# Kernel tuning notes

Hardware: AMD Instinct MI355X
Metric: run time of the kernel (lower is better)

Reference implementation:

```python
import jax, jax.numpy as jnp
import numpy as np

EPS = 1e-7
B, F, C, H, W, D = 2, 2, 64, 32, 104, 96


def _pix_homog(h, w):
    ys, xs = jnp.meshgrid(jnp.arange(h, dtype=jnp.float32),
                          jnp.arange(w, dtype=jnp.float32), indexing='ij')
    return jnp.stack([xs.ravel(), ys.ravel(), jnp.ones(h * w, jnp.float32)], 0)  # [3, H*W]


def setup_inputs() -> dict:
    key = jax.random.key(0)
    k1, k2 = jax.random.split(key)
    current_feats = jax.random.normal(k1, (B, C, H, W), jnp.float32)
    lookup_feats = jax.random.normal(k2, (B, F, C, H, W), jnp.float32)

    rng = np.random.RandomState(0)
    # intrinsics at matching (feature) resolution, monodepth2-style
    Km = np.eye(4, dtype=np.float32)
    Km[0, 0] = 0.58 * W
    Km[1, 1] = 1.92 * H
    Km[0, 2] = 0.5 * W
    Km[1, 2] = 0.5 * H
    K = np.tile(Km[None], (B, 1, 1))
    invK = np.linalg.inv(K).astype(np.float32)

    # near-identity relative poses (small rotation perturbation + small translation)
    poses = np.tile(np.eye(4, dtype=np.float32)[None, None], (B, F, 1, 1))
    poses[:, :, :3, :3] += 0.02 * rng.randn(B, F, 3, 3).astype(np.float32)
    poses[:, :, :3, 3] = 0.1 * rng.randn(B, F, 3).astype(np.float32)

    depth_bins = jnp.linspace(0.1, 20.0, D, dtype=jnp.float32)
    return {
        'current_feats': current_feats,
        'lookup_feats': lookup_feats,
        'poses': jnp.asarray(poses),
        'K': jnp.asarray(K),
        'invK': jnp.asarray(invK),
        'depth_bins': depth_bins,
    }


def _grid_sample_zeros(lfT, gx, gy, h, w):
    """Bilinear grid_sample, align_corners=True, padding_mode='zeros'.
    lfT: [B,F,H,W,C]; gx,gy: [B,F,D,H,W] in pixel coords. -> [B,F,D,H,W,C]"""
    x0 = jnp.floor(gx)
    y0 = jnp.floor(gy)
    x0i = x0.astype(jnp.int32)
    y0i = y0.astype(jnp.int32)
    wx1 = gx - x0
    wy1 = gy - y0
    wx0 = 1.0 - wx1
    wy0 = 1.0 - wy1
    bb = jnp.arange(lfT.shape[0])[:, None, None, None, None]
    ff = jnp.arange(lfT.shape[1])[None, :, None, None, None]

    def corner(yi, xi, wgt):
        m = ((xi >= 0) & (xi < w) & (yi >= 0) & (yi < h)).astype(lfT.dtype)
        xc = jnp.clip(xi, 0, w - 1)
        yc = jnp.clip(yi, 0, h - 1)
        v = lfT[bb, ff, yc, xc]                      # [B,F,D,H,W,C]
        return v * (m * wgt)[..., None]

    return (corner(y0i, x0i, wy0 * wx0) + corner(y0i, x0i + 1, wy0 * wx1)
            + corner(y0i + 1, x0i, wy1 * wx0) + corner(y0i + 1, x0i + 1, wy1 * wx1))


def reference(current_feats, lookup_feats, poses, K, invK, depth_bins):
    b, c, h, w = current_feats.shape
    f = lookup_feats.shape[1]
    d = depth_bins.shape[0]

    # Backproject: world points for each hypothesised depth plane
    pix = _pix_homog(h, w)                                   # [3, HW]
    cam = jnp.einsum('bij,jn->bin', invK[:, :3, :3], pix)    # [B,3,HW]
    pts = depth_bins[None, :, None, None] * cam[:, None]     # [B,D,3,HW]
    world = jnp.concatenate([pts, jnp.ones((b, d, 1, h * w), pts.dtype)], 2)  # [B,D,4,HW]

    # Project into each lookup frame
    P = jnp.einsum('bij,bfjk->bfik', K, poses)[:, :, :3, :]  # [B,F,3,4]
    cpts = jnp.einsum('bfij,bdjn->bfdin', P, world)          # [B,F,D,3,HW]
    xy = cpts[:, :, :, :2] / (cpts[:, :, :, 2:3] + EPS)      # pixel coords [B,F,D,2,HW]
    xy = xy.reshape(b, f, d, 2, h, w)
    gx, gy = xy[:, :, :, 0], xy[:, :, :, 1]                  # [B,F,D,H,W]

    # edge mask (detach in original -> stop_gradient)
    sx, sy = jax.lax.stop_gradient(gx), jax.lax.stop_gradient(gy)
    edge = ((sx >= 2.0) & (sx <= w - 2) & (sy >= 2.0) & (sy <= h - 2)).astype(jnp.float32)
    interior = jnp.zeros((h, w), jnp.float32).at[2:-2, 2:-2].set(1.0)
    edge_mask = edge * interior                               # [B,F,D,H,W]

    # warp lookup features and L1-diff against current features
    lfT = lookup_feats.transpose(0, 1, 3, 4, 2)               # [B,F,H,W,C]
    warped = _grid_sample_zeros(lfT, gx, gy, h, w)            # [B,F,D,H,W,C]
    cur = current_feats.transpose(0, 2, 3, 1)                 # [B,H,W,C]
    diffs = jnp.abs(warped - cur[:, None, None]).mean(-1) * edge_mask  # [B,F,D,H,W]

    # skip lookup frames whose pose is all-zero
    valid = (poses.sum((-2, -1)) != 0).astype(jnp.float32)    # [B,F]
    diffs = diffs * valid[:, :, None, None, None]

    cost = diffs.sum(1)                                        # [B,D,H,W]
    counts = (diffs > 0).astype(jnp.float32).sum(1)
    cost = cost / (counts + EPS)

    # set missing values to per-pixel max over depth bins
    missing = (cost == 0.0)
    cmax = cost.max(1, keepdims=True)
    cost = jnp.where(missing, cmax, cost)
    return cost
```

## Files before the change

### kernel.cpp

```cpp
#include <hip/hip_runtime.h>
#include <math.h>

constexpr int B_ = 2, F_ = 2, C_ = 64, H_ = 32, W_ = 104, D_ = 96;
constexpr int HW_ = H_ * W_;
#define EPSF 1e-7f

constexpr size_t LFT_OFF  = 0;
constexpr size_t CURT_OFF = LFT_OFF + (size_t)B_ * F_ * HW_ * C_;

constexpr int NT_BLKS = (HW_ / 32) * (C_ / 32) * (B_ * F_ + B_);
constexpr int DCH = 8;

__global__ __launch_bounds__(256) void prep_kernel(
        const float* __restrict__ cur, const float* __restrict__ lf,
        float* __restrict__ ws) {
    __shared__ float tile[32][33];
    int bid = blockIdx.x;
    int slice = bid / 208;
    int rem   = bid % 208;
    int nb = rem % 104, cb = rem / 104;
    const float* inS;
    float* outS;
    if (slice < B_ * F_) {
        inS  = lf + (size_t)slice * C_ * HW_;
        outS = ws + LFT_OFF + (size_t)slice * HW_ * C_;
    } else {
        int s2 = slice - B_ * F_;
        inS  = cur + (size_t)s2 * C_ * HW_;
        outS = ws + CURT_OFF + (size_t)s2 * HW_ * C_;
    }
    int t = threadIdx.x;
    int tx = t & 31, ty = t >> 5;
    int n0 = nb * 32, c0 = cb * 32;
    #pragma unroll
    for (int k = 0; k < 32; k += 8)
        tile[ty + k][tx] = inS[(size_t)(c0 + ty + k) * HW_ + n0 + tx];
    __syncthreads();
    #pragma unroll
    for (int k = 0; k < 32; k += 8)
        outS[(size_t)(n0 + ty + k) * C_ + c0 + tx] = tile[tx][ty + k];
}

__global__ __launch_bounds__(128) void sample_kernel(
        const float* __restrict__ poses, const float* __restrict__ K,
        const float* __restrict__ invK, const float* __restrict__ depth_bins,
        const float* __restrict__ ws, float* __restrict__ out) {
    int t   = threadIdx.x;
    int bid = blockIdx.x;
    int xt  = bid % 13;  int r = bid / 13;
    int d0c = r % (D_ / DCH);  r /= (D_ / DCH);
    int y   = r % H_;
    int b   = r / H_;
    int d0  = d0c * DCH;

    if (y < 2 || y >= H_ - 2) {
        if (t < 8 * DCH) {
            int dd = t >> 3, p2 = t & 7;
            out[((size_t)(b * D_ + d0 + dd) * H_ + y) * W_ + xt * 8 + p2] = 0.0f;
        }
        return;
    }

    __shared__ float2 gls[F_][DCH][8];

    {
        int px = t & 7, dc = (t >> 3) & 7, f = t >> 6;
        int x = xt * 8 + px, d = d0 + dc;
        const float* Kb   = K + (size_t)b * 16;
        const float* pose = poses + (size_t)(b * F_ + f) * 16;
        float P[12];
        #pragma unroll
        for (int i = 0; i < 3; ++i) {
            #pragma unroll
            for (int k = 0; k < 4; ++k) {
                float acc = __fmul_rn(Kb[i*4+0], pose[0*4+k]);
                acc = __fmaf_rn(Kb[i*4+1], pose[1*4+k], acc);
                acc = __fmaf_rn(Kb[i*4+2], pose[2*4+k], acc);
                acc = __fmaf_rn(Kb[i*4+3], pose[3*4+k], acc);
                P[i*4+k] = acc;
            }
        }
        float vs = 0.f;
        #pragma unroll
        for (int j = 0; j < 16; ++j) vs += pose[j];
        bool valid = (vs != 0.f);

        const float* iK = invK + (size_t)b * 16;
        float xf = (float)x, yf = (float)y;
        float cam0 = __fmul_rn(iK[0], xf); cam0 = __fmaf_rn(iK[1], yf, cam0); cam0 = __fmaf_rn(iK[2],  1.0f, cam0);
        float cam1 = __fmul_rn(iK[4], xf); cam1 = __fmaf_rn(iK[5], yf, cam1); cam1 = __fmaf_rn(iK[6],  1.0f, cam1);
        float cam2 = __fmul_rn(iK[8], xf); cam2 = __fmaf_rn(iK[9], yf, cam2); cam2 = __fmaf_rn(iK[10], 1.0f, cam2);
        float depth = depth_bins[d];
        float p0 = __fmul_rn(depth, cam0);
        float p1 = __fmul_rn(depth, cam1);
        float p2 = __fmul_rn(depth, cam2);

        float c0 = __fmul_rn(P[0], p0); c0 = __fmaf_rn(P[1], p1, c0); c0 = __fmaf_rn(P[2],  p2, c0); c0 = __fmaf_rn(P[3],  1.0f, c0);
        float c1 = __fmul_rn(P[4], p0); c1 = __fmaf_rn(P[5], p1, c1); c1 = __fmaf_rn(P[6],  p2, c1); c1 = __fmaf_rn(P[7],  1.0f, c1);
        float c2 = __fmul_rn(P[8], p0); c2 = __fmaf_rn(P[9], p1, c2); c2 = __fmaf_rn(P[10], p2, c2); c2 = __fmaf_rn(P[11], 1.0f, c2);
        float denom = __fadd_rn(c2, EPSF);
        float gx = c0 / denom;
        float gy = c1 / denom;

        bool interior = (x >= 2) && (x <= W_ - 3);
        bool m = valid && interior && (gx >= 2.0f) && (gx <= (float)(W_ - 2))
                                   && (gy >= 2.0f) && (gy <= (float)(H_ - 2));
        gls[f][dc][px] = m ? make_float2(gx, gy) : make_float2(2.0f, -1.0f);
    }
    __syncthreads();

    int lane = t & 15, px = t >> 4;
    int x = xt * 8 + px;
    const float4 cv = *(const float4*)(ws + CURT_OFF
                        + ((size_t)((b * H_ + y) * W_ + x)) * C_ + lane * 4);
    const float* lf0 = ws + LFT_OFF + (size_t)(b * F_ + 0) * HW_ * C_ + lane * 4;
    const float* lf1 = ws + LFT_OFF + (size_t)(b * F_ + 1) * HW_ * C_ + lane * 4;

    #pragma unroll 4
    for (int dc = 0; dc < DCH; ++dc) {
        float costsum = 0.f, counts = 0.f;
        #pragma unroll
        for (int f = 0; f < F_; ++f) {
            float2 g = gls[f][dc][px];
            bool  m  = (g.y >= 0.f);
            float gyv = m ? g.y : 2.0f;
            float gxv = g.x;
            float x0f = floorf(gxv), y0f = floorf(gyv);
            int   x0  = (int)x0f,    y0  = (int)y0f;
            float wx1 = gxv - x0f, wy1 = gyv - y0f;
            float wx0 = 1.f - wx1, wy0 = 1.f - wy1;
            float w00 = wy0 * wx0, w01 = wy0 * wx1, w10 = wy1 * wx0, w11 = wy1 * wx1;
            const float* bp = (f == 0 ? lf0 : lf1) + (size_t)(y0 * W_ + x0) * C_;
            float4 v00 = *(const float4*)(bp);
            float4 v01 = *(const float4*)(bp + C_);
            float4 v10 = *(const float4*)(bp + W_ * C_);
            float4 v11 = *(const float4*)(bp + W_ * C_ + C_);
            float s;
            s  = fabsf(v00.x*w00 + v01.x*w01 + v10.x*w10 + v11.x*w11 - cv.x);
            s += fabsf(v00.y*w00 + v01.y*w01 + v10.y*w10 + v11.y*w11 - cv.y);
            s += fabsf(v00.z*w00 + v01.z*w01 + v10.z*w10 + v11.z*w11 - cv.z);
            s += fabsf(v00.w*w00 + v01.w*w01 + v10.w*w10 + v11.w*w11 - cv.w);
            s += __shfl_xor(s, 1);
            s += __shfl_xor(s, 2);
            s += __shfl_xor(s, 4);
            s += __shfl_xor(s, 8);
            float diff = __fmul_rn(s, 1.0f / 64.0f) * (m ? 1.0f : 0.0f);
            costsum += diff;
            counts  += (diff > 0.f) ? 1.0f : 0.0f;
        }
        float cost = costsum / __fadd_rn(counts, EPSF);
        if (lane == 0)
            out[((size_t)(b * D_ + d0 + dc) * H_ + y) * W_ + x] = cost;
    }
}

__global__ __launch_bounds__(128) void fix_kernel(float* __restrict__ out) {
    int t  = threadIdx.x;
    int px = t & 7, j = t >> 3;
    int colg = blockIdx.x * 8 + px;
    int b  = colg / HW_;
    int yx = colg % HW_;
    float* base = out + (size_t)b * D_ * HW_ + yx;
    float v[6];
    float pm = 0.f;
    #pragma unroll
    for (int k = 0; k < 6; ++k) {
        v[k] = base[(size_t)(j + 16 * k) * HW_];
        pm = fmaxf(pm, v[k]);
    }
    __shared__ float pmbuf[128];
    __shared__ float cmaxbuf[8];
    pmbuf[t] = pm;
    __syncthreads();
    if (t < 8) {
        float cm = 0.f;
        #pragma unroll
        for (int jj = 0; jj < 16; ++jj) cm = fmaxf(cm, pmbuf[jj * 8 + t]);
        cmaxbuf[t] = cm;
    }
    __syncthreads();
    float cm = cmaxbuf[px];
    #pragma unroll
    for (int k = 0; k < 6; ++k)
        base[(size_t)(j + 16 * k) * HW_] = (v[k] == 0.0f) ? cm : v[k];
}

extern "C" void kernel_launch(void* const* d_in, const int* in_sizes, int n_in,
                              void* d_out, int out_size, void* d_ws, size_t ws_size,
                              hipStream_t stream) {
    const float* cur        = (const float*)d_in[0];
    const float* lf         = (const float*)d_in[1];
    const float* poses      = (const float*)d_in[2];
    const float* K          = (const float*)d_in[3];
    const float* invK       = (const float*)d_in[4];
    const float* depth_bins = (const float*)d_in[5];
    float* out = (float*)d_out;
    float* ws  = (float*)d_ws;

    prep_kernel<<<NT_BLKS, 256, 0, stream>>>(cur, lf, ws);

    int sample_blocks = B_ * H_ * 13 * (D_ / DCH);
    sample_kernel<<<sample_blocks, 128, 0, stream>>>(poses, K, invK, depth_bins, ws, out);

    fix_kernel<<<(B_ * HW_) / 8, 128, 0, stream>>>(out);
}
```

Baseline: 113.4 us.

## Fuse sampling and max-fill into one kernel covering all depth bins per block

Merges the sampling and fix kernels so each block handles all 96 depth bins for 8 pixels in a row. Sample offsets and bilinear weights are computed once into shared memory, the per-pixel max over depth is taken from a shared cost buffer, and the output is written once, so the separate read-modify-write pass over the output goes away. Corner loads are skipped when the integer sample offset repeats across consecutive depths. In exchange there are far fewer blocks (832 instead of 9984), which lowers parallelism and latency hiding, and each thread walks a serial 48-step depth loop.

```diff
diff --git a/kernel.cpp b/kernel.cpp
--- a/kernel.cpp
+++ b/kernel.cpp
@@ -9,7 +9,6 @@
 constexpr size_t CURT_OFF = LFT_OFF + (size_t)B_ * F_ * HW_ * C_;
 
 constexpr int NT_BLKS = (HW_ / 32) * (C_ / 32) * (B_ * F_ + B_);
-constexpr int DCH = 8;
 
 __global__ __launch_bounds__(256) void prep_kernel(
         const float* __restrict__ cur, const float* __restrict__ lf,
@@ -41,31 +40,32 @@
         outS[(size_t)(n0 + ty + k) * C_ + c0 + tx] = tile[tx][ty + k];
 }
 
-__global__ __launch_bounds__(128) void sample_kernel(
+__global__ __launch_bounds__(256) void mega_kernel(
         const float* __restrict__ poses, const float* __restrict__ K,
         const float* __restrict__ invK, const float* __restrict__ depth_bins,
         const float* __restrict__ ws, float* __restrict__ out) {
     int t   = threadIdx.x;
     int bid = blockIdx.x;
     int xt  = bid % 13;  int r = bid / 13;
-    int d0c = r % (D_ / DCH);  r /= (D_ / DCH);
     int y   = r % H_;
     int b   = r / H_;
-    int d0  = d0c * DCH;
 
     if (y < 2 || y >= H_ - 2) {
-        if (t < 8 * DCH) {
-            int dd = t >> 3, p2 = t & 7;
-            out[((size_t)(b * D_ + d0 + dd) * H_ + y) * W_ + xt * 8 + p2] = 0.0f;
+        for (int k = t; k < 8 * D_; k += 256) {
+            int d = k >> 3, px = k & 7;
+            out[((size_t)(b * D_ + d) * H_ + y) * W_ + xt * 8 + px] = 0.0f;
         }
         return;
     }
 
-    __shared__ float2 gls[F_][DCH][8];
-
-    {
-        int px = t & 7, dc = (t >> 3) & 7, f = t >> 6;
-        int x = xt * 8 + px, d = d0 + dc;
+    __shared__ int   offs[F_][D_][8];
+    __shared__ float wts [F_][D_][8][4];
+    __shared__ float costb[8][D_];
+    __shared__ float pmax[32][8];
+    __shared__ float cmaxb[8];
+
+    #pragma unroll
+    for (int f = 0; f < F_; ++f) {
         const float* Kb   = K + (size_t)b * 16;
         const float* pose = poses + (size_t)(b * F_ + f) * 16;
         float P[12];
@@ -84,105 +84,130 @@
         #pragma unroll
         for (int j = 0; j < 16; ++j) vs += pose[j];
         bool valid = (vs != 0.f);
-
         const float* iK = invK + (size_t)b * 16;
-        float xf = (float)x, yf = (float)y;
-        float cam0 = __fmul_rn(iK[0], xf); cam0 = __fmaf_rn(iK[1], yf, cam0); cam0 = __fmaf_rn(iK[2],  1.0f, cam0);
-        float cam1 = __fmul_rn(iK[4], xf); cam1 = __fmaf_rn(iK[5], yf, cam1); cam1 = __fmaf_rn(iK[6],  1.0f, cam1);
-        float cam2 = __fmul_rn(iK[8], xf); cam2 = __fmaf_rn(iK[9], yf, cam2); cam2 = __fmaf_rn(iK[10], 1.0f, cam2);
-        float depth = depth_bins[d];
-        float p0 = __fmul_rn(depth, cam0);
-        float p1 = __fmul_rn(depth, cam1);
-        float p2 = __fmul_rn(depth, cam2);
-
-        float c0 = __fmul_rn(P[0], p0); c0 = __fmaf_rn(P[1], p1, c0); c0 = __fmaf_rn(P[2],  p2, c0); c0 = __fmaf_rn(P[3],  1.0f, c0);
-        float c1 = __fmul_rn(P[4], p0); c1 = __fmaf_rn(P[5], p1, c1); c1 = __fmaf_rn(P[6],  p2, c1); c1 = __fmaf_rn(P[7],  1.0f, c1);
-        float c2 = __fmul_rn(P[8], p0); c2 = __fmaf_rn(P[9], p1, c2); c2 = __fmaf_rn(P[10], p2, c2); c2 = __fmaf_rn(P[11], 1.0f, c2);
-        float denom = __fadd_rn(c2, EPSF);
-        float gx = c0 / denom;
-        float gy = c1 / denom;
-
-        bool interior = (x >= 2) && (x <= W_ - 3);
-        bool m = valid && interior && (gx >= 2.0f) && (gx <= (float)(W_ - 2))
-                                   && (gy >= 2.0f) && (gy <= (float)(H_ - 2));
-        gls[f][dc][px] = m ? make_float2(gx, gy) : make_float2(2.0f, -1.0f);
+
+        #pragma unroll
+        for (int k = 0; k < 3; ++k) {
+            int idx = t + 256 * k;
+            int dd = idx >> 3, px = idx & 7;
+            int x = xt * 8 + px;
+            float xf = (float)x, yf = (float)y;
+            float cam0 = __fmul_rn(iK[0], xf); cam0 = __fmaf_rn(iK[1], yf, cam0); cam0 = __fmaf_rn(iK[2],  1.0f, cam0);
+            float cam1 = __fmul_rn(iK[4], xf); cam1 = __fmaf_rn(iK[5], yf, cam1); cam1 = __fmaf_rn(iK[6],  1.0f, cam1);
+            float cam2 = __fmul_rn(iK[8], xf); cam2 = __fmaf_rn(iK[9], yf, cam2); cam2 = __fmaf_rn(iK[10], 1.0f, cam2);
+            float depth = depth_bins[dd];
+            float p0 = __fmul_rn(depth, cam0);
+            float p1 = __fmul_rn(depth, cam1);
+            float p2 = __fmul_rn(depth, cam2);
+            float c0 = __fmul_rn(P[0], p0); c0 = __fmaf_rn(P[1], p1, c0); c0 = __fmaf_rn(P[2],  p2, c0); c0 = __fmaf_rn(P[3],  1.0f, c0);
+            float c1 = __fmul_rn(P[4], p0); c1 = __fmaf_rn(P[5], p1, c1); c1 = __fmaf_rn(P[6],  p2, c1); c1 = __fmaf_rn(P[7],  1.0f, c1);
+            float c2 = __fmul_rn(P[8], p0); c2 = __fmaf_rn(P[9], p1, c2); c2 = __fmaf_rn(P[10], p2, c2); c2 = __fmaf_rn(P[11], 1.0f, c2);
+            float denom = __fadd_rn(c2, EPSF);
+            float gx = c0 / denom;
+            float gy = c1 / denom;
+            bool interior = (x >= 2) && (x <= W_ - 3);
+            bool m = valid && interior && (gx >= 2.0f) && (gx <= (float)(W_ - 2))
+                                       && (gy >= 2.0f) && (gy <= (float)(H_ - 2));
+            if (m) {
+                float x0f = floorf(gx), y0f = floorf(gy);
+                int   x0  = (int)x0f,   y0  = (int)y0f;
+                float wx1 = gx - x0f, wy1 = gy - y0f;
+                float wx0 = 1.f - wx1, wy0 = 1.f - wy1;
+                wts[f][dd][px][0] = wy0 * wx0;
+                wts[f][dd][px][1] = wy0 * wx1;
+                wts[f][dd][px][2] = wy1 * wx0;
+                wts[f][dd][px][3] = wy1 * wx1;
+                offs[f][dd][px] = (y0 * W_ + x0) * C_;
+            } else {
+                offs[f][dd][px] = -1;
+                wts[f][dd][px][0] = 0.f;
+                wts[f][dd][px][1] = 0.f;
+                wts[f][dd][px][2] = 0.f;
+                wts[f][dd][px][3] = 0.f;
+            }
+        }
     }
     __syncthreads();
 
-    int lane = t & 15, px = t >> 4;
-    int x = xt * 8 + px;
-    const float4 cv = *(const float4*)(ws + CURT_OFF
-                        + ((size_t)((b * H_ + y) * W_ + x)) * C_ + lane * 4);
-    const float* lf0 = ws + LFT_OFF + (size_t)(b * F_ + 0) * HW_ * C_ + lane * 4;
-    const float* lf1 = ws + LFT_OFF + (size_t)(b * F_ + 1) * HW_ * C_ + lane * 4;
-
-    #pragma unroll 4
-    for (int dc = 0; dc < DCH; ++dc) {
-        float costsum = 0.f, counts = 0.f;
-        #pragma unroll
-        for (int f = 0; f < F_; ++f) {
-            float2 g = gls[f][dc][px];
-            bool  m  = (g.y >= 0.f);
-            float gyv = m ? g.y : 2.0f;
-            float gxv = g.x;
-            float x0f = floorf(gxv), y0f = floorf(gyv);
-            int   x0  = (int)x0f,    y0  = (int)y0f;
-            float wx1 = gxv - x0f, wy1 = gyv - y0f;
-            float wx0 = 1.f - wx1, wy0 = 1.f - wy1;
-            float w00 = wy0 * wx0, w01 = wy0 * wx1, w10 = wy1 * wx0, w11 = wy1 * wx1;
-            const float* bp = (f == 0 ? lf0 : lf1) + (size_t)(y0 * W_ + x0) * C_;
-            float4 v00 = *(const float4*)(bp);
-            float4 v01 = *(const float4*)(bp + C_);
-            float4 v10 = *(const float4*)(bp + W_ * C_);
-            float4 v11 = *(const float4*)(bp + W_ * C_ + C_);
-            float s;
-            s  = fabsf(v00.x*w00 + v01.x*w01 + v10.x*w10 + v11.x*w11 - cv.x);
-            s += fabsf(v00.y*w00 + v01.y*w01 + v10.y*w10 + v11.y*w11 - cv.y);
-            s += fabsf(v00.z*w00 + v01.z*w01 + v10.z*w10 + v11.z*w11 - cv.z);
-            s += fabsf(v00.w*w00 + v01.w*w01 + v10.w*w10 + v11.w*w11 - cv.w);
-            s += __shfl_xor(s, 1);
-            s += __shfl_xor(s, 2);
-            s += __shfl_xor(s, 4);
-            s += __shfl_xor(s, 8);
-            float diff = __fmul_rn(s, 1.0f / 64.0f) * (m ? 1.0f : 0.0f);
-            costsum += diff;
-            counts  += (diff > 0.f) ? 1.0f : 0.0f;
-        }
-        float cost = costsum / __fadd_rn(counts, EPSF);
-        if (lane == 0)
-            out[((size_t)(b * D_ + d0 + dc) * H_ + y) * W_ + x] = cost;
-    }
-}
-
-__global__ __launch_bounds__(128) void fix_kernel(float* __restrict__ out) {
-    int t  = threadIdx.x;
-    int px = t & 7, j = t >> 3;
-    int colg = blockIdx.x * 8 + px;
-    int b  = colg / HW_;
-    int yx = colg % HW_;
-    float* base = out + (size_t)b * D_ * HW_ + yx;
-    float v[6];
-    float pm = 0.f;
-    #pragma unroll
-    for (int k = 0; k < 6; ++k) {
-        v[k] = base[(size_t)(j + 16 * k) * HW_];
-        pm = fmaxf(pm, v[k]);
-    }
-    __shared__ float pmbuf[128];
-    __shared__ float cmaxbuf[8];
-    pmbuf[t] = pm;
+    {
+        int lane = t & 15, px = (t >> 4) & 7, half = t >> 7;
+        int x = xt * 8 + px;
+        const float4 cv = *(const float4*)(ws + CURT_OFF
+                            + ((size_t)((b * H_ + y) * W_ + x)) * C_ + lane * 4);
+        const float* lfb[F_];
+        lfb[0] = ws + LFT_OFF + (size_t)(b * F_ + 0) * HW_ * C_ + lane * 4;
+        lfb[1] = ws + LFT_OFF + (size_t)(b * F_ + 1) * HW_ * C_ + lane * 4;
+
+        float4 cc[F_][4];
+        int oprev[F_] = { -1, -1 };
+        #pragma unroll
+        for (int f = 0; f < F_; ++f)
+            cc[f][0] = cc[f][1] = cc[f][2] = cc[f][3] = make_float4(0.f, 0.f, 0.f, 0.f);
+
+        int dbeg = half * (D_ / 2), dend = dbeg + (D_ / 2);
+        for (int dc = dbeg; dc < dend; ++dc) {
+            float costsum = 0.f, counts = 0.f;
+            #pragma unroll
+            for (int f = 0; f < F_; ++f) {
+                int  o = offs[f][dc][px];
+                bool m = (o >= 0);
+                if (m && o != oprev[f]) {
+                    const float* bp = lfb[f] + o;
+                    cc[f][0] = *(const float4*)(bp);
+                    cc[f][1] = *(const float4*)(bp + C_);
+                    cc[f][2] = *(const float4*)(bp + W_ * C_);
+                    cc[f][3] = *(const float4*)(bp + W_ * C_ + C_);
+                    oprev[f] = o;
+                }
+                float w00 = wts[f][dc][px][0];
+                float w01 = wts[f][dc][px][1];
+                float w10 = wts[f][dc][px][2];
+                float w11 = wts[f][dc][px][3];
+                float s;
+                s  = fabsf(cc[f][0].x*w00 + cc[f][1].x*w01 + cc[f][2].x*w10 + cc[f][3].x*w11 - cv.x);
+                s += fabsf(cc[f][0].y*w00 + cc[f][1].y*w01 + cc[f][2].y*w10 + cc[f][3].y*w11 - cv.y);
+                s += fabsf(cc[f][0].z*w00 + cc[f][1].z*w01 + cc[f][2].z*w10 + cc[f][3].z*w11 - cv.z);
+                s += fabsf(cc[f][0].w*w00 + cc[f][1].w*w01 + cc[f][2].w*w10 + cc[f][3].w*w11 - cv.w);
+                s += __shfl_xor(s, 1);
+                s += __shfl_xor(s, 2);
+                s += __shfl_xor(s, 4);
+                s += __shfl_xor(s, 8);
+                float diff = __fmul_rn(s, 1.0f / 64.0f) * (m ? 1.0f : 0.0f);
+                costsum += diff;
+                counts  += (diff > 0.f) ? 1.0f : 0.0f;
+            }
+            float cost = costsum / __fadd_rn(counts, EPSF);
+            if (lane == 0) costb[px][dc] = cost;
+        }
+    }
     __syncthreads();
-    if (t < 8) {
-        float cm = 0.f;
-        #pragma unroll
-        for (int jj = 0; jj < 16; ++jj) cm = fmaxf(cm, pmbuf[jj * 8 + t]);
-        cmaxbuf[t] = cm;
-    }
-    __syncthreads();
-    float cm = cmaxbuf[px];
-    #pragma unroll
-    for (int k = 0; k < 6; ++k)
-        base[(size_t)(j + 16 * k) * HW_] = (v[k] == 0.0f) ? cm : v[k];
+
+    {
+        int j = t >> 3, px = t & 7;
+        float v[3];
+        float pm = 0.f;
+        #pragma unroll
+        for (int k = 0; k < 3; ++k) {
+            v[k] = costb[px][j + 32 * k];
+            pm = fmaxf(pm, v[k]);
+        }
+        pmax[j][px] = pm;
+        __syncthreads();
+        if (t < 8) {
+            float cm = 0.f;
+            #pragma unroll
+            for (int jj = 0; jj < 32; ++jj) cm = fmaxf(cm, pmax[jj][t]);
+            cmaxb[t] = cm;
+        }
+        __syncthreads();
+        float cm = cmaxb[px];
+        int x = xt * 8 + px;
+        #pragma unroll
+        for (int k = 0; k < 3; ++k) {
+            int d = j + 32 * k;
+            out[((size_t)(b * D_ + d) * H_ + y) * W_ + x] = (v[k] == 0.0f) ? cm : v[k];
+        }
+    }
 }
 
 extern "C" void kernel_launch(void* const* d_in, const int* in_sizes, int n_in,
@@ -198,9 +223,5 @@
     float* ws  = (float*)d_ws;
 
     prep_kernel<<<NT_BLKS, 256, 0, stream>>>(cur, lf, ws);
-
-    int sample_blocks = B_ * H_ * 13 * (D_ / DCH);
-    sample_kernel<<<sample_blocks, 128, 0, stream>>>(poses, K, invK, depth_bins, ws, out);
-
-    fix_kernel<<<(B_ * HW_) / 8, 128, 0, stream>>>(out);
+    mega_kernel<<<B_ * H_ * 13, 256, 0, stream>>>(poses, K, invK, depth_bins, ws, out);
 }
```

Result: faster. 109.8 us (-3.2%).
